# Performance work log

Hardware: AMD Instinct MI355X
Metric: run time of the kernel (lower is better)

Reference implementation:

```python
import jax, jax.numpy as jnp
import numpy as np

B, K, N, L = 4096, 64, 100000, 256  # queries, neighbors, exemplars, label dim


def setup_inputs() -> dict:
    key = jax.random.key(0)
    k1, k2, k3, k4, k5 = jax.random.split(key, 5)
    tau_squared = jnp.float32(1.0)
    n_train = jnp.float32(1_000_000)
    return {
        "sq_dists": jax.random.uniform(k1, (B, K), dtype=jnp.float32) * 2.0,
        "labels": jax.random.randint(k2, (B, K), 0, N, dtype=jnp.int64),
        "exemplar_labels": jax.random.uniform(k3, (N, L), dtype=jnp.float32),
        "exemplar_sizes": jax.random.uniform(k4, (N,), dtype=jnp.float32) * 10.0 + 1.0,
        "average_label": jax.random.uniform(k5, (L,), dtype=jnp.float32),
        "tau_squared": tau_squared,
        "gamma_n": jnp.exp(-tau_squared) / n_train,
    }


def reference(sq_dists, labels, exemplar_labels, exemplar_sizes, average_label,
              tau_squared, gamma_n):
    # Sparse kNN kernel weights: exp(-d^2) truncated at tau^2.  [B, K]
    w = jnp.exp(-sq_dists) * (sq_dists <= tau_squared).astype(sq_dists.dtype)
    # Gather-weighted reduce == dense csr.toarray() @ exemplar_labels, since
    # duplicate (row, col) entries sum in both formulations.
    gathered = exemplar_labels[labels]            # [B, K, L]
    numer = jnp.einsum("bk,bkl->bl", w, gathered) + gamma_n * average_label
    denom = jnp.einsum("bk,bk->b", w, exemplar_sizes[labels])[:, None] + gamma_n
    return numer / denom                          # [B, L]
```

## Files before the change

kernel.cpp:

```cpp
#include <hip/hip_runtime.h>
#include <hip/hip_bf16.h>

#define BQ 4096
#define KN 64
#define LD 256
#define QPB 4

__global__ __launch_bounds__(256) void knn_weighted_gather_kernel(
    const float* __restrict__ sq_dists,
    const int*   __restrict__ labels,
    const float* __restrict__ exemplar_labels,
    const float* __restrict__ exemplar_sizes,
    const float* __restrict__ average_label,
    const float* __restrict__ tau_squared_p,
    const float* __restrict__ gamma_n_p,
    float* __restrict__ out)
{
    const int wave = threadIdx.x >> 6;
    const int lane = threadIdx.x & 63;
    const int q    = blockIdx.x * QPB + wave;

    const float tau2    = tau_squared_p[0];
    const float gamma_n = gamma_n_p[0];

    float d   = sq_dists[q * KN + lane];
    int   lab = labels  [q * KN + lane];
    float w   = (d <= tau2) ? __expf(-d) : 0.0f;

    float dpart = w * exemplar_sizes[lab];
    #pragma unroll
    for (int off = 32; off > 0; off >>= 1)
        dpart += __shfl_xor(dpart, off, 64);

    unsigned long long mask = __ballot(w != 0.0f);
    const int nact = __popcll(mask);
    const int wbits = __float_as_int(w);
    const float* __restrict__ colbase = exemplar_labels + lane * 4;

    float4 acc = make_float4(0.f, 0.f, 0.f, 0.f);

#define STEP(SV, WV, LV, VV)                                          \
    int SV = (int)__builtin_ctzll(mask); mask &= mask - 1;            \
    float WV = __int_as_float(__builtin_amdgcn_readlane(wbits, SV));  \
    int LV = __builtin_amdgcn_readlane(lab, SV);                      \
    const float4 VV = *reinterpret_cast<const float4*>(colbase + (size_t)LV * LD)

#define FMA4(WV, VV)                                                  \
    acc.x += WV * VV.x; acc.y += WV * VV.y;                           \
    acc.z += WV * VV.z; acc.w += WV * VV.w

    int i = 0;
    for (; i + 8 <= nact; i += 8) {
        STEP(s0, w0, l0, v0); STEP(s1, w1, l1, v1);
        STEP(s2, w2, l2, v2); STEP(s3, w3, l3, v3);
        STEP(s4, w4, l4, v4); STEP(s5, w5, l5, v5);
        STEP(s6, w6, l6, v6); STEP(s7, w7, l7, v7);
        FMA4(w0, v0); FMA4(w1, v1); FMA4(w2, v2); FMA4(w3, v3);
        FMA4(w4, v4); FMA4(w5, v5); FMA4(w6, v6); FMA4(w7, v7);
    }
    for (; i < nact; ++i) {
        STEP(s0, w0, l0, v0);
        FMA4(w0, v0);
    }
#undef STEP
#undef FMA4

    const float4 avg = *reinterpret_cast<const float4*>(average_label + lane * 4);
    const float inv = 1.0f / (dpart + gamma_n);
    float4 res;
    res.x = (acc.x + gamma_n * avg.x) * inv;
    res.y = (acc.y + gamma_n * avg.y) * inv;
    res.z = (acc.z + gamma_n * avg.z) * inv;
    res.w = (acc.w + gamma_n * avg.w) * inv;
    *reinterpret_cast<float4*>(out + (size_t)q * LD + lane * 4) = res;
}

extern "C" void kernel_launch(void* const* d_in, const int* in_sizes, int n_in,
                              void* d_out, int out_size, void* d_ws, size_t ws_size,
                              hipStream_t stream) {
    const float* sq_dists        = (const float*)d_in[0];
    const int*   labels          = (const int*)  d_in[1];
    const float* exemplar_labels = (const float*)d_in[2];
    const float* exemplar_sizes  = (const float*)d_in[3];
    const float* average_label   = (const float*)d_in[4];
    const float* tau_squared     = (const float*)d_in[5];
    const float* gamma_n         = (const float*)d_in[6];
    float* out = (float*)d_out;

    knn_weighted_gather_kernel<<<BQ / QPB, QPB * 64, 0, stream>>>(
        sq_dists, labels, exemplar_labels, exemplar_sizes, average_label,
        tau_squared, gamma_n, out);
}
```

Before: 27.30 us.

## Split each query's neighbor set across two waves and reduce through LDS

Each query is now handled by two waves, each covering half of the 64 neighbors. Partial accumulators and denominators are combined through shared memory after a block barrier. This doubles the wave count and shortens each wave's serial gather chain, aiming for more memory-level parallelism. The cost is an extra LDS reduction, a __syncthreads, and an occupancy hint in launch_bounds.

```diff
diff --git a/kernel.cpp b/kernel.cpp
--- a/kernel.cpp
+++ b/kernel.cpp
@@ -3,10 +3,10 @@
 
 #define BQ 4096
 #define KN 64
+#define KH 32
 #define LD 256
-#define QPB 4
 
-__global__ __launch_bounds__(256) void knn_weighted_gather_kernel(
+__global__ __launch_bounds__(256, 8) void knn_weighted_gather_kernel(
     const float* __restrict__ sq_dists,
     const int*   __restrict__ labels,
     const float* __restrict__ exemplar_labels,
@@ -16,23 +16,29 @@
     const float* __restrict__ gamma_n_p,
     float* __restrict__ out)
 {
+    __shared__ float4 s_acc[2][64];
+    __shared__ float  s_den[2];
+
     const int wave = threadIdx.x >> 6;
     const int lane = threadIdx.x & 63;
-    const int q    = blockIdx.x * QPB + wave;
+    const int qloc = wave >> 1;
+    const int h    = wave & 1;
+    const int q    = blockIdx.x * 2 + qloc;
 
     const float tau2    = tau_squared_p[0];
     const float gamma_n = gamma_n_p[0];
 
-    float d   = sq_dists[q * KN + lane];
-    int   lab = labels  [q * KN + lane];
+    const int kk = h * KH + (lane & (KH - 1));
+    float d   = sq_dists[q * KN + kk];
+    int   lab = labels  [q * KN + kk];
     float w   = (d <= tau2) ? __expf(-d) : 0.0f;
 
     float dpart = w * exemplar_sizes[lab];
     #pragma unroll
-    for (int off = 32; off > 0; off >>= 1)
+    for (int off = KH / 2; off > 0; off >>= 1)
         dpart += __shfl_xor(dpart, off, 64);
 
-    unsigned long long mask = __ballot(w != 0.0f);
+    unsigned long long mask = __ballot(w != 0.0f) & 0xFFFFFFFFull;
     const int nact = __popcll(mask);
     const int wbits = __float_as_int(w);
     const float* __restrict__ colbase = exemplar_labels + lane * 4;
@@ -65,14 +71,24 @@
 #undef STEP
 #undef FMA4
 
-    const float4 avg = *reinterpret_cast<const float4*>(average_label + lane * 4);
-    const float inv = 1.0f / (dpart + gamma_n);
-    float4 res;
-    res.x = (acc.x + gamma_n * avg.x) * inv;
-    res.y = (acc.y + gamma_n * avg.y) * inv;
-    res.z = (acc.z + gamma_n * avg.z) * inv;
-    res.w = (acc.w + gamma_n * avg.w) * inv;
-    *reinterpret_cast<float4*>(out + (size_t)q * LD + lane * 4) = res;
+    if (h == 1) {
+        s_acc[qloc][lane] = acc;
+        if (lane == 0) s_den[qloc] = dpart;
+    }
+    __syncthreads();
+    if (h == 0) {
+        const float4 o = s_acc[qloc][lane];
+        acc.x += o.x; acc.y += o.y; acc.z += o.z; acc.w += o.w;
+        const float den = dpart + s_den[qloc] + gamma_n;
+        const float inv = 1.0f / den;
+        const float4 avg = *reinterpret_cast<const float4*>(average_label + lane * 4);
+        float4 res;
+        res.x = (acc.x + gamma_n * avg.x) * inv;
+        res.y = (acc.y + gamma_n * avg.y) * inv;
+        res.z = (acc.z + gamma_n * avg.z) * inv;
+        res.w = (acc.w + gamma_n * avg.w) * inv;
+        *reinterpret_cast<float4*>(out + (size_t)q * LD + lane * 4) = res;
+    }
 }
 
 extern "C" void kernel_launch(void* const* d_in, const int* in_sizes, int n_in,
@@ -87,7 +103,7 @@
     const float* gamma_n         = (const float*)d_in[6];
     float* out = (float*)d_out;
 
-    knn_weighted_gather_kernel<<<BQ / QPB, QPB * 64, 0, stream>>>(
+    knn_weighted_gather_kernel<<<BQ / 2, 256, 0, stream>>>(
         sq_dists, labels, exemplar_labels, exemplar_sizes, average_label,
         tau_squared, gamma_n, out);
 }
```

Measured after the change: 26.99 us (median of 2 runs). About the same (-1.1%).
